# Kernel tuning notes

Hardware: AMD Instinct MI355X
Metric: run time of the kernel (lower is better)

The kernel has to match this reference:

```python
import jax, jax.numpy as jnp
import numpy as np

NUM_HEADS = 8
EPS = 1e-3

N_TOKENS = 32768
DIM = 256
N_WIN = 128
WIN = N_TOKENS // N_WIN  # 256 tokens per window


def setup_inputs() -> dict:
    key = jax.random.key(0)
    ks = jax.random.split(key, 4)
    x = jax.random.normal(ks[0], (N_TOKENS, DIM), dtype=jnp.float32)
    # torch nn.Linear weights are [out_features, in_features]
    w_qkv = jax.random.normal(ks[1], (3 * DIM, DIM), dtype=jnp.float32) * (DIM ** -0.5)
    w_proj = jax.random.normal(ks[2], (DIM, DIM), dtype=jnp.float32) * (DIM ** -0.5)
    b_proj = jnp.zeros((DIM,), dtype=jnp.float32)
    batch_win_inds = (jnp.arange(N_TOKENS) // WIN).astype(jnp.int64)
    offsets = (jnp.arange(N_WIN) * WIN).astype(jnp.int64)
    counts = jnp.full((N_WIN,), WIN, dtype=jnp.int64)
    return {"x": x, "w_qkv": w_qkv, "w_proj": w_proj, "b_proj": b_proj,
            "offsets": offsets, "counts": counts, "batch_win_inds": batch_win_inds}


def reference(x, w_qkv, w_proj, b_proj, offsets, counts, batch_win_inds):
    N, C = x.shape
    H = NUM_HEADS
    hd = C // H
    W = counts.shape[0]  # number of windows (static)

    qkv = x @ w_qkv.T                      # [N, 3C]
    q, k, v = jnp.split(qkv, 3, axis=-1)   # each [N, C]
    q = jax.nn.relu(q.reshape(N, H, hd))   # [N, H, hd]
    k = jax.nn.relu(k.reshape(N, H, hd))
    v = v.reshape(N, H, hd)

    seg = batch_win_inds.astype(jnp.int32)
    # per-window KV state: kv[w] = sum_{i in w} k_i^T v_i   -> [W, H, hd, hd]
    kv = jax.ops.segment_sum(jnp.einsum('nhc,nhd->nhcd', k, v), seg, num_segments=W)
    # per-window key sum for normalizer                      -> [W, H, hd]
    s = jax.ops.segment_sum(k, seg, num_segments=W)

    y = jnp.einsum('nhc,nhcd->nhd', q, kv[seg])              # [N, H, hd]
    z = jnp.sum(s[seg] * q, axis=-1, keepdims=True)          # [N, H, 1]
    y = y / (z + EPS)

    y = y.reshape(N, C) @ w_proj.T + b_proj                  # [N, C]
    return y
```

## Files before the change

kernel.cpp:

```cpp
#include <hip/hip_runtime.h>

typedef __bf16 bf16_t;
typedef bf16_t bf16x8 __attribute__((ext_vector_type(8)));
typedef bf16_t bf16x4 __attribute__((ext_vector_type(4)));
typedef float f32x4 __attribute__((ext_vector_type(4)));

#define M_TOK 32768
#define NWIN 128
#define WIN  256

typedef __attribute__((address_space(3))) void* as3p;
typedef const __attribute__((address_space(1))) void* as1p;

__device__ __forceinline__ void gll16(const void* g, void* l) {
    __builtin_amdgcn_global_load_lds((as1p)g, (as3p)l, 16, 0, 0);
}

__device__ __forceinline__ bf16x8 cvt8(f32x4 a, f32x4 b) {
    bf16x8 o;
    o[0] = (bf16_t)a[0]; o[1] = (bf16_t)a[1]; o[2] = (bf16_t)a[2]; o[3] = (bf16_t)a[3];
    o[4] = (bf16_t)b[0]; o[5] = (bf16_t)b[1]; o[6] = (bf16_t)b[2]; o[7] = (bf16_t)b[3];
    return o;
}

#define VMW_(n) asm volatile("s_waitcnt vmcnt(" #n ")" ::: "memory")
#define VMW(n) VMW_(n)
#define LGKM0 asm volatile("s_waitcnt lgkmcnt(0)" ::: "memory")

#define MFMA16(b, a, c) __builtin_amdgcn_mfma_f32_16x16x32_bf16((b), (a), (c), 0, 0, 0)

__global__ __launch_bounds__(256) void wconv(
    const float* __restrict__ wq, const float* __restrict__ wp,
    bf16_t* __restrict__ wqb, bf16_t* __restrict__ wpb)
{
    int i4 = (blockIdx.x * 256 + threadIdx.x) * 4;
    const float* s; bf16_t* dst; int idx;
    if (i4 < 196608) { s = wq; dst = wqb; idx = i4; }
    else             { s = wp; dst = wpb; idx = i4 - 196608; }
    f32x4 v = *(const f32x4*)(s + idx);
    bf16x4 o;
    o[0] = (bf16_t)v[0]; o[1] = (bf16_t)v[1]; o[2] = (bf16_t)v[2]; o[3] = (bf16_t)v[3];
    *(bf16x4*)(dst + idx) = o;
}

__global__ __launch_bounds__(512) void fused_attn(
    const float* __restrict__ X,
    const bf16_t* __restrict__ Wq,
    const int* __restrict__ offsets,
    const int* __restrict__ counts,
    bf16_t* __restrict__ Y)
{
    __shared__ __align__(16) bf16_t Wl2[2][96 * 256];
    __shared__ __align__(16) bf16_t KT[32 * 256];
    __shared__ __align__(16) bf16_t VT[32 * 256];
    __shared__ __align__(16) bf16_t Ql[256 * 40];
    __shared__ __align__(16) bf16_t kvb[32 * 32];
    __shared__ float sfp[32];
    __shared__ float zin[256];

    const int bid = blockIdx.x;
    const int w  = (bid & 7) * 16 + (bid >> 4);
    const int hh = (bid >> 3) & 1;
    const int is64 = (counts[1] == 0) ? 1 : 0;
    const int off = offsets[w << is64];
    const int tid = threadIdx.x;
    const int lane = tid & 63;
    const int wv = tid >> 6;
    const int r = lane & 15, q = lane >> 4;

    auto stageW = [&](int h, int buf) {
#pragma unroll
        for (int u = 0; u < 6; ++u) {
            const int rl = wv * 12 + u * 2 + (lane >> 5);
            const int grow = (rl < 32 ? 256 + rl : (rl < 64 ? 480 + rl : rl - 64)) + h * 32;
            gll16(Wq + (size_t)grow * 256 + ((lane & 31) ^ (rl & 7)) * 8,
                  &Wl2[buf][(wv * 12 + u * 2) * 256]);
        }
    };

    stageW(hh * 4, 0);
    bf16x8 xr[2][8];
#pragma unroll
    for (int i2 = 0; i2 < 2; ++i2) {
        const float* xp = X + (size_t)(off + wv * 32 + i2 * 16 + r) * 256 + q * 8;
#pragma unroll
        for (int kch = 0; kch < 8; ++kch) {
            f32x4 lo = *(const f32x4*)(xp + kch * 32);
            f32x4 hi = *(const f32x4*)(xp + kch * 32 + 4);
            xr[i2][kch] = cvt8(lo, hi);
        }
    }

    for (int h4 = 0; h4 < 4; ++h4) {
        const int h = hh * 4 + h4;
        const int buf = h4 & 1;
        VMW(0);
        __builtin_amdgcn_s_barrier();
        __builtin_amdgcn_sched_barrier(0);
        const bf16_t* Wl = &Wl2[buf][0];

        f32x4 aQ[2][2] = {}, aK[2][2] = {}, aV[2][2] = {};
#pragma unroll
        for (int kch = 0; kch < 8; ++kch) {
            const int slot8 = (((kch * 4 + q) ^ (r & 7)) * 8);
#pragma unroll
            for (int ct = 0; ct < 2; ++ct) {
                bf16x8 bk = *(const bf16x8*)(Wl + (ct * 16 + r) * 256 + slot8);
                bf16x8 bv = *(const bf16x8*)(Wl + (32 + ct * 16 + r) * 256 + slot8);
                bf16x8 bq = *(const bf16x8*)(Wl + (64 + ct * 16 + r) * 256 + slot8);
#pragma unroll
                for (int i2 = 0; i2 < 2; ++i2) {
                    aQ[i2][ct] = MFMA16(bq, xr[i2][kch], aQ[i2][ct]);
                    aK[i2][ct] = MFMA16(bk, xr[i2][kch], aK[i2][ct]);
                    aV[i2][ct] = MFMA16(bv, xr[i2][kch], aV[i2][ct]);
                }
            }
        }
        if (h4 < 3) stageW(h + 1, buf ^ 1);

#pragma unroll
        for (int i2 = 0; i2 < 2; ++i2) {
            const int t = wv * 32 + i2 * 16 + r;
            const int gt = t >> 3;
#pragma unroll
            for (int ct = 0; ct < 2; ++ct)
#pragma unroll
                for (int reg = 0; reg < 4; ++reg) {
                    const int c = ct * 16 + q * 4 + reg;
                    const int ei = c * 256 + (gt ^ (c & 7)) * 8 + (t & 7);
                    KT[ei] = (bf16_t)fmaxf(aK[i2][ct][reg], 0.f);
                    VT[ei] = (bf16_t)aV[i2][ct][reg];
                }
        }
        LGKM0;
        __builtin_amdgcn_s_barrier();
        __builtin_amdgcn_sched_barrier(0);

        f32x4 kva = {};
        float sc = 0.f;
        if (wv < 4) {
            const int ct = wv >> 1, dt = wv & 1;
#pragma unroll
            for (int kch = 0; kch < 8; ++kch) {
                const int slot8 = (((kch * 4 + q) ^ (r & 7)) * 8);
                bf16x8 ak = *(const bf16x8*)(KT + (ct * 16 + r) * 256 + slot8);
                bf16x8 bv2 = *(const bf16x8*)(VT + (dt * 16 + r) * 256 + slot8);
                kva = MFMA16(bv2, ak, kva);
            }
        } else {
            const int tl = tid - 256;
            const int c = tl >> 3, p = tl & 7;
#pragma unroll
            for (int g = 0; g < 4; ++g) {
                bf16x8 kk = *(const bf16x8*)(KT + c * 256 + (p + g * 8) * 8);
#pragma unroll
                for (int j = 0; j < 8; ++j) sc += (float)kk[j];
            }
            sc += __shfl_xor(sc, 1);
            sc += __shfl_xor(sc, 2);
            sc += __shfl_xor(sc, 4);
        }

#pragma unroll
        for (int i2 = 0; i2 < 2; ++i2) {
            const int t = wv * 32 + i2 * 16 + r;
#pragma unroll
            for (int ct = 0; ct < 2; ++ct) {
                bf16x4 o;
#pragma unroll
                for (int reg = 0; reg < 4; ++reg)
                    o[reg] = (bf16_t)fmaxf(aQ[i2][ct][reg], 0.f);
                *(bf16x4*)(Ql + t * 40 + ct * 16 + q * 4) = o;
            }
        }
        if (wv < 4) {
            const int ct = wv >> 1, dt = wv & 1;
#pragma unroll
            for (int reg = 0; reg < 4; ++reg)
                kvb[(dt * 16 + q * 4 + reg) * 32 + ct * 16 + r] = (bf16_t)kva[reg];
        } else {
            const int tl = tid - 256;
            if ((tl & 7) == 0) sfp[tl >> 3] = sc;
        }
        LGKM0;
        __builtin_amdgcn_s_barrier();
        __builtin_amdgcn_sched_barrier(0);

        if (tid < 256) {
            float z = 0.f;
#pragma unroll
            for (int g = 0; g < 4; ++g) {
                bf16x8 qq = *(const bf16x8*)(Ql + tid * 40 + g * 8);
#pragma unroll
                for (int j = 0; j < 8; ++j) z += (float)qq[j] * sfp[g * 8 + j];
            }
            zin[tid] = 1.f / (z + 1e-3f);
        }
        LGKM0;
        __builtin_amdgcn_s_barrier();
        __builtin_amdgcn_sched_barrier(0);

        {
            bf16x8 bk0 = *(const bf16x8*)(kvb + r * 32 + q * 8);
            bf16x8 bk1 = *(const bf16x8*)(kvb + (16 + r) * 32 + q * 8);
#pragma unroll
            for (int i2 = 0; i2 < 2; ++i2) {
                const int t = wv * 32 + i2 * 16 + r;
                bf16x8 aq = *(const bf16x8*)(Ql + t * 40 + q * 8);
                f32x4 y0 = {}, y1 = {};
                y0 = MFMA16(bk0, aq, y0);
                y1 = MFMA16(bk1, aq, y1);
                const float zi = zin[t];
                bf16x4 o0, o1;
#pragma unroll
                for (int reg = 0; reg < 4; ++reg) {
                    o0[reg] = (bf16_t)(y0[reg] * zi);
                    o1[reg] = (bf16_t)(y1[reg] * zi);
                }
                bf16_t* yp = Y + (size_t)(off + t) * 256 + h * 32;
                *(bf16x4*)(yp + q * 4) = o0;
                *(bf16x4*)(yp + 16 + q * 4) = o1;
            }
        }
    }
}

__global__ __launch_bounds__(512) void gemm2_proj(
    const bf16_t* __restrict__ Y,
    const bf16_t* __restrict__ Wb,
    const float* __restrict__ bias,
    float* __restrict__ Out)
{
    __shared__ __align__(16) bf16_t Al[64][256];
    __shared__ __align__(16) bf16_t Bs[3][128][64];

    const int tid = threadIdx.x;
    const int lane = tid & 63;
    const int wv = tid >> 6;
    const int wm = wv >> 2, wn = wv & 3;
    const int m0 = blockIdx.x * 64;
    const int r = lane & 15, q = lane >> 4;
    const int rl = lane >> 3, gsl = lane & 7;

    f32x4 acc[2][2] = {};

    auto stageB = [&](int t) {
        const int nb = t >> 2, kc = (t & 3) * 64;
#pragma unroll
        for (int u = 0; u < 2; ++u)
            gll16(Wb + (size_t)(nb * 128 + wv * 16 + u * 8 + rl) * 256 + kc + (gsl ^ rl) * 8,
                  &Bs[t % 3][wv * 16 + u * 8][0]);
    };

    auto comp = [&](int t) {
        const int buf = t % 3;
#pragma unroll
        for (int s = 0; s < 2; ++s) {
            const int kk = (t & 3) * 2 + s;
            bf16x8 a[2], b[2];
#pragma unroll
            for (int i = 0; i < 2; ++i)
                a[i] = *(const bf16x8*)((const bf16_t*)Al +
                        (wm * 32 + i * 16 + r) * 256 + ((kk * 4 + q) ^ (r & 7)) * 8);
#pragma unroll
            for (int j = 0; j < 2; ++j)
                b[j] = *(const bf16x8*)&Bs[buf][wn * 32 + j * 16 + r][((s * 4 + q) ^ (r & 7)) * 8];
#pragma unroll
            for (int i = 0; i < 2; ++i)
#pragma unroll
                for (int j = 0; j < 2; ++j)
                    acc[i][j] = MFMA16(b[j], a[i], acc[i][j]);
        }
    };

    auto wout = [&](int nb) {
#pragma unroll
        for (int i = 0; i < 2; ++i) {
            const int rowg = m0 + wm * 32 + i * 16 + r;
#pragma unroll
            for (int j = 0; j < 2; ++j) {
                const int n = nb * 128 + wn * 32 + j * 16 + q * 4;
                f32x4 bi = *(const f32x4*)(bias + n);
                f32x4 o;
#pragma unroll
                for (int reg = 0; reg < 4; ++reg) o[reg] = acc[i][j][reg] + bi[reg];
                *(f32x4*)&Out[(size_t)rowg * 256 + n] = o;
                acc[i][j] = (f32x4){0.f, 0.f, 0.f, 0.f};
            }
        }
    };

#pragma unroll
    for (int u = 0; u < 4; ++u) {
        const int rowl = wv * 8 + u * 2 + (lane >> 5);
        const int gsrc = (lane & 31) ^ (rowl & 7);
        gll16(Y + (size_t)(m0 + rowl) * 256 + gsrc * 8, &Al[wv * 8 + u * 2][0]);
    }
    stageB(0); stageB(1); stageB(2);

#define G2S(t, NW) do { \
        VMW(NW); \
        __builtin_amdgcn_s_barrier(); \
        __builtin_amdgcn_sched_barrier(0); \
        comp(t); \
        if (((t) & 3) == 3) wout((t) >> 2); \
        __builtin_amdgcn_sched_barrier(0); \
        __builtin_amdgcn_s_barrier(); \
        if ((t) + 3 < 8) stageB((t) + 3); \
    } while (0)

    G2S(0, 4); G2S(1, 4); G2S(2, 4); G2S(3, 4);
    G2S(4, 4); G2S(5, 4); G2S(6, 2); G2S(7, 0);
#undef G2S
}

extern "C" void kernel_launch(void* const* d_in, const int* in_sizes, int n_in,
                              void* d_out, int out_size, void* d_ws, size_t ws_size,
                              hipStream_t stream) {
    const float* x      = (const float*)d_in[0];
    const float* w_qkv  = (const float*)d_in[1];
    const float* w_proj = (const float*)d_in[2];
    const float* b_proj = (const float*)d_in[3];
    const int*   offs   = (const int*)d_in[4];
    const int*   cnts   = (const int*)d_in[5];

    char* ws = (char*)d_ws;
    bf16_t* Y   = (bf16_t*)(ws + 50331648);
    bf16_t* Wqb = (bf16_t*)(ws + 67108864);
    bf16_t* Wpb = (bf16_t*)(ws + 67502080);
    float*  out = (float*)d_out;

    wconv<<<256, 256, 0, stream>>>(w_qkv, w_proj, Wqb, Wpb);

    fused_attn<<<256, 512, 0, stream>>>(x, Wqb, offs, cnts, Y);

    gemm2_proj<<<512, 512, 0, stream>>>(Y, Wpb, b_proj, out);
}
```

Before: 129.6 us.

## Split heads across more blocks, shrink LDS, compute Q path in registers

The fused attention kernel now launches 512 blocks, each handling 2 heads instead of 4. W staging drops to a single K/V buffer, and Q weights are read directly from global memory, which cuts LDS use and targets higher occupancy (launch bounds min 4 blocks). The Q tile and normalizer no longer go through LDS: z is reduced with lane shuffles and the Q operand is rearranged into MFMA layout via shuffles, which removes one barrier and the Ql/zin buffers. The trade-off is that X is reloaded and converted twice as often, and Q weight reads now come from global/L2.

```diff
diff --git a/kernel.cpp b/kernel.cpp
--- a/kernel.cpp
+++ b/kernel.cpp
@@ -4,6 +4,7 @@
 typedef bf16_t bf16x8 __attribute__((ext_vector_type(8)));
 typedef bf16_t bf16x4 __attribute__((ext_vector_type(4)));
 typedef float f32x4 __attribute__((ext_vector_type(4)));
+typedef unsigned int u32;
 
 #define M_TOK 32768
 #define NWIN 128
@@ -43,24 +44,22 @@
     *(bf16x4*)(dst + idx) = o;
 }
 
-__global__ __launch_bounds__(512) void fused_attn(
+__global__ __launch_bounds__(512, 4) void fused_attn(
     const float* __restrict__ X,
     const bf16_t* __restrict__ Wq,
     const int* __restrict__ offsets,
     const int* __restrict__ counts,
     bf16_t* __restrict__ Y)
 {
-    __shared__ __align__(16) bf16_t Wl2[2][96 * 256];
+    __shared__ __align__(16) bf16_t Wl[64 * 256];
     __shared__ __align__(16) bf16_t KT[32 * 256];
     __shared__ __align__(16) bf16_t VT[32 * 256];
-    __shared__ __align__(16) bf16_t Ql[256 * 40];
     __shared__ __align__(16) bf16_t kvb[32 * 32];
-    __shared__ float sfp[32];
-    __shared__ float zin[256];
+    __shared__ __align__(16) float sfp[32];
 
     const int bid = blockIdx.x;
-    const int w  = (bid & 7) * 16 + (bid >> 4);
-    const int hh = (bid >> 3) & 1;
+    const int w  = (bid & 7) * 16 + ((bid >> 3) & 15);
+    const int hp = bid >> 7;
     const int is64 = (counts[1] == 0) ? 1 : 0;
     const int off = offsets[w << is64];
     const int tid = threadIdx.x;
@@ -68,17 +67,17 @@
     const int wv = tid >> 6;
     const int r = lane & 15, q = lane >> 4;
 
-    auto stageW = [&](int h, int buf) {
-#pragma unroll
-        for (int u = 0; u < 6; ++u) {
-            const int rl = wv * 12 + u * 2 + (lane >> 5);
-            const int grow = (rl < 32 ? 256 + rl : (rl < 64 ? 480 + rl : rl - 64)) + h * 32;
+    auto stageW = [&](int h) {
+#pragma unroll
+        for (int u = 0; u < 4; ++u) {
+            const int rl = wv * 8 + u * 2 + (lane >> 5);
+            const int grow = (rl < 32 ? 256 + rl : 480 + rl) + h * 32;
             gll16(Wq + (size_t)grow * 256 + ((lane & 31) ^ (rl & 7)) * 8,
-                  &Wl2[buf][(wv * 12 + u * 2) * 256]);
+                  &Wl[(wv * 8 + u * 2) * 256]);
         }
     };
 
-    stageW(hh * 4, 0);
+    stageW(hp * 2);
     bf16x8 xr[2][8];
 #pragma unroll
     for (int i2 = 0; i2 < 2; ++i2) {
@@ -91,13 +90,11 @@
         }
     }
 
-    for (int h4 = 0; h4 < 4; ++h4) {
-        const int h = hh * 4 + h4;
-        const int buf = h4 & 1;
+    for (int h4 = 0; h4 < 2; ++h4) {
+        const int h = hp * 2 + h4;
         VMW(0);
         __builtin_amdgcn_s_barrier();
         __builtin_amdgcn_sched_barrier(0);
-        const bf16_t* Wl = &Wl2[buf][0];
 
         f32x4 aQ[2][2] = {}, aK[2][2] = {}, aV[2][2] = {};
 #pragma unroll
@@ -107,7 +104,8 @@
             for (int ct = 0; ct < 2; ++ct) {
                 bf16x8 bk = *(const bf16x8*)(Wl + (ct * 16 + r) * 256 + slot8);
                 bf16x8 bv = *(const bf16x8*)(Wl + (32 + ct * 16 + r) * 256 + slot8);
-                bf16x8 bq = *(const bf16x8*)(Wl + (64 + ct * 16 + r) * 256 + slot8);
+                bf16x8 bq = *(const bf16x8*)(Wq + (size_t)(h * 32 + ct * 16 + r) * 256
+                                              + kch * 32 + q * 8);
 #pragma unroll
                 for (int i2 = 0; i2 < 2; ++i2) {
                     aQ[i2][ct] = MFMA16(bq, xr[i2][kch], aQ[i2][ct]);
@@ -116,7 +114,6 @@
                 }
             }
         }
-        if (h4 < 3) stageW(h + 1, buf ^ 1);
 
 #pragma unroll
         for (int i2 = 0; i2 < 2; ++i2) {
@@ -135,10 +132,10 @@
         LGKM0;
         __builtin_amdgcn_s_barrier();
         __builtin_amdgcn_sched_barrier(0);
-
-        f32x4 kva = {};
-        float sc = 0.f;
+        if (h4 == 0) stageW(h + 1);
+
         if (wv < 4) {
+            f32x4 kva = {};
             const int ct = wv >> 1, dt = wv & 1;
 #pragma unroll
             for (int kch = 0; kch < 8; ++kch) {
@@ -147,7 +144,11 @@
                 bf16x8 bv2 = *(const bf16x8*)(VT + (dt * 16 + r) * 256 + slot8);
                 kva = MFMA16(bv2, ak, kva);
             }
+#pragma unroll
+            for (int reg = 0; reg < 4; ++reg)
+                kvb[(dt * 16 + q * 4 + reg) * 32 + ct * 16 + r] = (bf16_t)kva[reg];
         } else {
+            float sc = 0.f;
             const int tl = tid - 256;
             const int c = tl >> 3, p = tl & 7;
 #pragma unroll
@@ -159,63 +160,64 @@
             sc += __shfl_xor(sc, 1);
             sc += __shfl_xor(sc, 2);
             sc += __shfl_xor(sc, 4);
-        }
-
-#pragma unroll
-        for (int i2 = 0; i2 < 2; ++i2) {
-            const int t = wv * 32 + i2 * 16 + r;
-#pragma unroll
-            for (int ct = 0; ct < 2; ++ct) {
-                bf16x4 o;
-#pragma unroll
-                for (int reg = 0; reg < 4; ++reg)
-                    o[reg] = (bf16_t)fmaxf(aQ[i2][ct][reg], 0.f);
-                *(bf16x4*)(Ql + t * 40 + ct * 16 + q * 4) = o;
-            }
-        }
-        if (wv < 4) {
-            const int ct = wv >> 1, dt = wv & 1;
-#pragma unroll
-            for (int reg = 0; reg < 4; ++reg)
-                kvb[(dt * 16 + q * 4 + reg) * 32 + ct * 16 + r] = (bf16_t)kva[reg];
-        } else {
-            const int tl = tid - 256;
             if ((tl & 7) == 0) sfp[tl >> 3] = sc;
         }
         LGKM0;
         __builtin_amdgcn_s_barrier();
         __builtin_amdgcn_sched_barrier(0);
 
-        if (tid < 256) {
-            float z = 0.f;
-#pragma unroll
-            for (int g = 0; g < 4; ++g) {
-                bf16x8 qq = *(const bf16x8*)(Ql + tid * 40 + g * 8);
-#pragma unroll
-                for (int j = 0; j < 8; ++j) z += (float)qq[j] * sfp[g * 8 + j];
-            }
-            zin[tid] = 1.f / (z + 1e-3f);
-        }
-        LGKM0;
-        __builtin_amdgcn_s_barrier();
-        __builtin_amdgcn_sched_barrier(0);
+        bf16x8 qa[2];
+        float zi[2];
+#pragma unroll
+        for (int i2 = 0; i2 < 2; ++i2) {
+            bf16x4 o0, o1;
+            float qb0[4], qb1[4];
+#pragma unroll
+            for (int reg = 0; reg < 4; ++reg) {
+                o0[reg] = (bf16_t)fmaxf(aQ[i2][0][reg], 0.f);
+                o1[reg] = (bf16_t)fmaxf(aQ[i2][1][reg], 0.f);
+                qb0[reg] = (float)o0[reg];
+                qb1[reg] = (float)o1[reg];
+            }
+            f32x4 s0 = *(const f32x4*)&sfp[q * 4];
+            f32x4 s1 = *(const f32x4*)&sfp[16 + q * 4];
+            float zz = 0.f;
+#pragma unroll
+            for (int reg = 0; reg < 4; ++reg)
+                zz += qb0[reg] * s0[reg] + qb1[reg] * s1[reg];
+            zz += __shfl_xor(zz, 16);
+            zz += __shfl_xor(zz, 32);
+            zi[i2] = 1.f / (zz + 1e-3f);
+            u32 p0x, p0y, p1x, p1y;
+            { uint2 t0 = *(uint2*)&o0; p0x = t0.x; p0y = t0.y; }
+            { uint2 t1 = *(uint2*)&o1; p1x = t1.x; p1y = t1.y; }
+            const int sl0 = r + 16 * (2 * (q & 1));
+            const int sl1 = sl0 + 16;
+            u32 a0 = __shfl((int)p0x, sl0), a1 = __shfl((int)p0y, sl0);
+            u32 a2 = __shfl((int)p0x, sl1), a3 = __shfl((int)p0y, sl1);
+            u32 b0 = __shfl((int)p1x, sl0), b1 = __shfl((int)p1y, sl0);
+            u32 b2 = __shfl((int)p1x, sl1), b3 = __shfl((int)p1y, sl1);
+            u32 wq4[4];
+            const bool hi = (q >> 1) != 0;
+            wq4[0] = hi ? b0 : a0; wq4[1] = hi ? b1 : a1;
+            wq4[2] = hi ? b2 : a2; wq4[3] = hi ? b3 : a3;
+            qa[i2] = *(bf16x8*)wq4;
+        }
 
         {
             bf16x8 bk0 = *(const bf16x8*)(kvb + r * 32 + q * 8);
             bf16x8 bk1 = *(const bf16x8*)(kvb + (16 + r) * 32 + q * 8);
 #pragma unroll
             for (int i2 = 0; i2 < 2; ++i2) {
+                f32x4 y0 = {}, y1 = {};
+                y0 = MFMA16(bk0, qa[i2], y0);
+                y1 = MFMA16(bk1, qa[i2], y1);
                 const int t = wv * 32 + i2 * 16 + r;
-                bf16x8 aq = *(const bf16x8*)(Ql + t * 40 + q * 8);
-                f32x4 y0 = {}, y1 = {};
-                y0 = MFMA16(bk0, aq, y0);
-                y1 = MFMA16(bk1, aq, y1);
-                const float zi = zin[t];
                 bf16x4 o0, o1;
 #pragma unroll
                 for (int reg = 0; reg < 4; ++reg) {
-                    o0[reg] = (bf16_t)(y0[reg] * zi);
-                    o1[reg] = (bf16_t)(y1[reg] * zi);
+                    o0[reg] = (bf16_t)(y0[reg] * zi[i2]);
+                    o1[reg] = (bf16_t)(y1[reg] * zi[i2]);
                 }
                 bf16_t* yp = Y + (size_t)(off + t) * 256 + h * 32;
                 *(bf16x4*)(yp + q * 4) = o0;
@@ -332,7 +334,7 @@
 
     wconv<<<256, 256, 0, stream>>>(w_qkv, w_proj, Wqb, Wpb);
 
-    fused_attn<<<256, 512, 0, stream>>>(x, Wqb, offs, cnts, Y);
+    fused_attn<<<512, 512, 0, stream>>>(x, Wqb, offs, cnts, Y);
 
     gemm2_proj<<<512, 512, 0, stream>>>(Y, Wpb, b_proj, out);
 }
```

New measurement: 169.8 us. 31.0% more time.
